# Kernel tuning notes

Hardware: AMD Instinct MI355X
Metric: run time of the kernel (lower is better)

Reference implementation:

```python
import jax, jax.numpy as jnp
import numpy as np

# NOTE: create_positions() is not defined in the source repo snippet. We implement the
# standard duration-model convention: per-frame offset within its phoneme segment,
# i.e. positions[b,t] = t - start_frame(segment containing t). mode is unused here.

B, N, T, D = 8, 512, 8192, 256


def setup_inputs() -> dict:
    key = jax.random.key(0)
    rng = np.random.default_rng(0)
    dur = rng.integers(8, 24, size=(B, N)).astype(np.int64)
    # force every row to sum exactly to T so max(sum(durations)) == T (static shape)
    dur[:, -1] += T - dur.sum(axis=1)
    assert (dur > 0).all()
    durations = jnp.asarray(dur, dtype=jnp.int32)
    x = jax.random.normal(key, (B, N, D), dtype=jnp.float32)
    return {"x": x, "durations": durations}


def reference(x, durations):
    durf = durations.astype(jnp.float32)                      # [B,N]
    e = jnp.cumsum(durf, axis=-1)                             # segment end frames [B,N]
    c = e - 0.5 * durf                                        # segment centers   [B,N]
    # T is static by construction (rows of durations all sum to the same total)
    t = jnp.arange(T, dtype=jnp.float32)                      # [T]
    # weights[b,n,t] = 1 iff |t - c + 1e-6| < dur/2 (zeros-then-fill in torch == this)
    w = jnp.abs(t[None, None, :] - c[:, :, None] + 1e-6)      # [B,N,T]
    weights = (w < durf[:, :, None] * 0.5).astype(jnp.float32)
    # out[b,t,d] = sum_n weights[b,n,t] * x[b,n,d]  (== weights.transpose(1,2) @ x)
    out = jnp.einsum('bnt,bnd->btd', weights, x)              # [B,T,D]
    # create_positions: offset of each frame within its phoneme segment
    starts = e - durf                                         # [B,N]
    positions = t[None, :] - jnp.einsum('bnt,bn->bt', weights, starts)  # [B,T]
    return positions, out, weights
```

## Files before the change

### kernel.cpp

```cpp
#include <hip/hip_runtime.h>
#include <math.h>

#define BB 8
#define NN 512
#define TT 8192
#define DD 256

#define THREADS 256
#define BLOCKS  512
#define FRAMES  128
#define MAXROWS 18

typedef float v4f __attribute__((ext_vector_type(4)));

__global__ void __launch_bounds__(THREADS)
fused_kernel(const float* __restrict__ x,
             const int* __restrict__ dur,
             float* __restrict__ positions,
             float* __restrict__ outp,
             float* __restrict__ w) {
    __shared__ int s_end[NN + 1];
    __shared__ unsigned char s_cov[NN];
    __shared__ int s_ps[THREADS];
    __shared__ short seg_blk[FRAMES];
    __shared__ int s_nlo, s_nhi;
    __shared__ float xs[(MAXROWS + 1) * DD];

    const int bid = blockIdx.x;
    const int b   = bid >> 6;
    const int sub = bid & 63;
    const int tid = threadIdx.x;

    const int2 dp = *(const int2*)(dur + b * NN + 2 * tid);
    s_ps[tid] = dp.x + dp.y;
    for (int off = 1; off < THREADS; off <<= 1) {
        __syncthreads();
        const int v = (tid >= off) ? s_ps[tid - off] : 0;
        __syncthreads();
        s_ps[tid] += v;
    }
    const int S = s_ps[tid];
    if (tid == 0) s_end[0] = 0;
    s_end[2 * tid + 1] = S - dp.y;
    s_end[2 * tid + 2] = S;
    {
        const float h0 = 0.5f * (float)dp.x;
        const float h1 = 0.5f * (float)dp.y;
        s_cov[2 * tid]     = (fabsf(1e-6f - h0) < h0) ? 1 : 0;
        s_cov[2 * tid + 1] = (fabsf(1e-6f - h1) < h1) ? 1 : 0;
    }
    __syncthreads();

    const int f0 = sub * FRAMES;
    if (tid < FRAMES) {
        const int t = f0 + tid;
        int lo = 0, hi = NN - 1;
        while (lo < hi) {
            const int mid = (lo + hi) >> 1;
            if (t < s_end[mid + 1]) hi = mid; else lo = mid + 1;
        }
        const int st   = s_end[lo];
        const bool unc = (t == st) && !s_cov[lo];
        seg_blk[tid] = (short)(unc ? -1 : lo);
        positions[b * TT + t] = unc ? (float)t : (float)(t - st);
        if (tid == 0)          s_nlo = lo;
        if (tid == FRAMES - 1) s_nhi = lo;
    }
    __syncthreads();

    const int nlo   = s_nlo;
    const int nrows = s_nhi - nlo + 1;
    for (int idx = tid; idx < (nrows + 1) * (DD / 4); idx += THREADS) {
        const int r  = idx >> 6;
        const int d4 = (idx & 63) << 2;
        v4f v = (v4f)(0.0f);
        if (r < nrows)
            v = *(const v4f*)(x + (((size_t)b * NN + nlo + r) * DD + d4));
        *(v4f*)(xs + r * DD + d4) = v;
    }
    __syncthreads();

    float* oc = outp + ((size_t)b * TT + f0) * DD;
    #pragma unroll 4
    for (int k = 0; k < FRAMES * (DD / 4) / THREADS; ++k) {
        const int idx = k * THREADS + tid;
        const int f   = idx >> 6;
        const int d4  = (idx & 63) << 2;
        const int sg  = seg_blk[f];
        const int row = (sg < 0) ? nrows : (sg - nlo);
        const v4f v = *(const v4f*)(xs + row * DD + d4);
        __builtin_nontemporal_store(v, (v4f*)(oc + ((size_t)idx << 2)));
    }

    const int n0 = sub * 8;
    for (int r = 0; r < 8; ++r) {
        const int n  = n0 + r;
        const int rs = s_end[n] + (s_cov[n] ? 0 : 1);
        const int re = s_end[n + 1];
        float* wrow = w + (((size_t)b * NN + n) << 13);
        for (int t = rs + tid; t < re; t += THREADS)
            wrow[t] = 1.0f;
    }
}

extern "C" void kernel_launch(void* const* d_in, const int* in_sizes, int n_in,
                              void* d_out, int out_size, void* d_ws, size_t ws_size,
                              hipStream_t stream) {
    const float* x  = (const float*)d_in[0];
    const int* dur  = (const int*)d_in[1];

    float* pos  = (float*)d_out;
    float* outp = pos + (size_t)BB * TT;
    float* w    = outp + (size_t)BB * TT * DD;

    hipMemsetAsync(w, 0, (size_t)BB * NN * TT * sizeof(float), stream);
    fused_kernel<<<BLOCKS, THREADS, 0, stream>>>(x, dur, pos, outp, w);
}
```

Baseline: 39.92 us.

## Fold weight zero-fill into kernel with dense vector stores; use wavefront prefix scan

The separate hipMemsetAsync over the full weights tensor is removed. Each block now writes its eight full weight rows itself with 16-byte nontemporal stores, computing 0/1 per element from the segment bounds. This drops the extra pass that zeroed the buffer before a second, scattered pass wrote the ones. The block-wide shared-memory prefix sum of durations is replaced by a single-wavefront shuffle scan, with each lane summing 8 durations, which removes many barriers.

```diff
diff --git a/kernel.cpp b/kernel.cpp
--- a/kernel.cpp
+++ b/kernel.cpp
@@ -21,33 +21,38 @@
              float* __restrict__ w) {
     __shared__ int s_end[NN + 1];
     __shared__ unsigned char s_cov[NN];
-    __shared__ int s_ps[THREADS];
     __shared__ short seg_blk[FRAMES];
     __shared__ int s_nlo, s_nhi;
     __shared__ float xs[(MAXROWS + 1) * DD];
 
-    const int bid = blockIdx.x;
-    const int b   = bid >> 6;
-    const int sub = bid & 63;
-    const int tid = threadIdx.x;
+    const int bid  = blockIdx.x;
+    const int b    = bid >> 6;
+    const int sub  = bid & 63;
+    const int tid  = threadIdx.x;
+    const int lane = tid & 63;
 
-    const int2 dp = *(const int2*)(dur + b * NN + 2 * tid);
-    s_ps[tid] = dp.x + dp.y;
-    for (int off = 1; off < THREADS; off <<= 1) {
-        __syncthreads();
-        const int v = (tid >= off) ? s_ps[tid - off] : 0;
-        __syncthreads();
-        s_ps[tid] += v;
-    }
-    const int S = s_ps[tid];
-    if (tid == 0) s_end[0] = 0;
-    s_end[2 * tid + 1] = S - dp.y;
-    s_end[2 * tid + 2] = S;
-    {
-        const float h0 = 0.5f * (float)dp.x;
-        const float h1 = 0.5f * (float)dp.y;
-        s_cov[2 * tid]     = (fabsf(1e-6f - h0) < h0) ? 1 : 0;
-        s_cov[2 * tid + 1] = (fabsf(1e-6f - h1) < h1) ? 1 : 0;
+    if (tid < 64) {
+        const int4 da = *(const int4*)(dur + b * NN + 8 * lane);
+        const int4 db = *(const int4*)(dur + b * NN + 8 * lane + 4);
+        int d[8] = {da.x, da.y, da.z, da.w, db.x, db.y, db.z, db.w};
+        int pre[8], s = 0;
+        #pragma unroll
+        for (int j = 0; j < 8; ++j) { pre[j] = s; s += d[j]; }
+        int incl = s;
+        #pragma unroll
+        for (int off = 1; off < 64; off <<= 1) {
+            const int v = __shfl_up(incl, off, 64);
+            if (lane >= off) incl += v;
+        }
+        const int base = incl - s;
+        #pragma unroll
+        for (int j = 0; j < 8; ++j) {
+            const int n = 8 * lane + j;
+            s_end[n] = base + pre[j];
+            const float h = 0.5f * (float)d[j];
+            s_cov[n] = (fabsf(1e-6f - h) < h) ? 1 : 0;
+        }
+        if (lane == 63) s_end[NN] = incl;
     }
     __syncthreads();
 
@@ -93,13 +98,22 @@
     }
 
     const int n0 = sub * 8;
+    #pragma unroll
     for (int r = 0; r < 8; ++r) {
         const int n  = n0 + r;
         const int rs = s_end[n] + (s_cov[n] ? 0 : 1);
         const int re = s_end[n + 1];
         float* wrow = w + (((size_t)b * NN + n) << 13);
-        for (int t = rs + tid; t < re; t += THREADS)
-            wrow[t] = 1.0f;
+        #pragma unroll
+        for (int k = 0; k < 8; ++k) {
+            const int t = (k * THREADS + tid) << 2;
+            v4f o;
+            o.x = (t     >= rs && t     < re) ? 1.0f : 0.0f;
+            o.y = (t + 1 >= rs && t + 1 < re) ? 1.0f : 0.0f;
+            o.z = (t + 2 >= rs && t + 2 < re) ? 1.0f : 0.0f;
+            o.w = (t + 3 >= rs && t + 3 < re) ? 1.0f : 0.0f;
+            __builtin_nontemporal_store(o, (v4f*)(wrow + t));
+        }
     }
 }
 
@@ -113,6 +127,5 @@
     float* outp = pos + (size_t)BB * TT;
     float* w    = outp + (size_t)BB * TT * DD;
 
-    hipMemsetAsync(w, 0, (size_t)BB * NN * TT * sizeof(float), stream);
     fused_kernel<<<BLOCKS, THREADS, 0, stream>>>(x, dur, pos, outp, w);
 }
```

New measurement: 43.03 us. +7.8%, slower.
